# Kernel optimization log

Hardware: AMD Instinct MI355X
Metric: run time of the kernel (lower is better)

Reference implementation:

```python
import jax, jax.numpy as jnp
import numpy as np

N = 50000      # nodes per graph
E = 800000     # edges per graph (avg degree 16)
IN = 128       # in_channels == hidden_channels
HID = 128      # out_channels (heads=1)
R = 8          # num_relations
NEG = 0.2      # PyG RGATConv default negative_slope


def setup_inputs() -> dict:
    key = jax.random.key(0)
    ks = jax.random.split(key, 14)
    s_w = (2.0 / (IN + HID)) ** 0.5  # glorot-ish scale
    return {
        "x_one": jax.random.normal(ks[0], (N, IN), jnp.float32),
        "edge_index_one": jax.random.randint(ks[1], (2, E), 0, N),
        "edge_type_one": jax.random.randint(ks[2], (E,), 0, R),
        "x_two": jax.random.normal(ks[3], (N, IN), jnp.float32),
        "edge_index_two": jax.random.randint(ks[4], (2, E), 0, N),
        "edge_type_two": jax.random.randint(ks[5], (E,), 0, R),
        "W1": jax.random.normal(ks[6], (R, IN, HID), jnp.float32) * s_w,
        "q1": jax.random.normal(ks[7], (HID, 1), jnp.float32) * s_w,
        "k1": jax.random.normal(ks[8], (HID, 1), jnp.float32) * s_w,
        "b1": jnp.zeros((HID,), jnp.float32),
        "W2": jax.random.normal(ks[9], (R, IN, HID), jnp.float32) * s_w,
        "q2": jax.random.normal(ks[10], (HID, 1), jnp.float32) * s_w,
        "k2": jax.random.normal(ks[11], (HID, 1), jnp.float32) * s_w,
        "b2": jnp.zeros((HID,), jnp.float32),
    }


def _rgat(x, edge_index, edge_type, W, q, k, b):
    """PyG RGATConv (heads=1, additive-self-attention, across-relation)."""
    n = x.shape[0]
    src, dst = edge_index[0], edge_index[1]
    # per-relation linear transform of all nodes: [R, N, HID]
    xt = jnp.einsum('nd,rdo->rno', x, W)
    out_i = xt[edge_type, dst]   # [E, HID] transformed target (x_i W_r)
    out_j = xt[edge_type, src]   # [E, HID] transformed source (x_j W_r)
    qi = out_i @ q               # [E, 1]
    kj = out_j @ k               # [E, 1]
    alpha = jax.nn.leaky_relu(qi + kj, NEG)
    # scatter-softmax over incoming edges of each dst node
    amax = jax.ops.segment_max(alpha, dst, num_segments=n)
    amax = jnp.where(jnp.isfinite(amax), amax, 0.0)
    ex = jnp.exp(alpha - amax[dst])
    denom = jax.ops.segment_sum(ex, dst, num_segments=n) + 1e-16
    a = ex / denom[dst]          # [E, 1]
    # weighted scatter-add aggregation + bias
    out = jax.ops.segment_sum(a * out_j, dst, num_segments=n) + b
    return out


def reference(x_one, edge_index_one, edge_type_one,
              x_two, edge_index_two, edge_type_two,
              W1, q1, k1, b1, W2, q2, k2, b2):
    o1 = jax.nn.relu(_rgat(x_one, edge_index_one, edge_type_one, W1, q1, k1, b1))
    o2 = jax.nn.relu(_rgat(x_two, edge_index_two, edge_type_two, W2, q2, k2, b2))
    return (o1, o2)
```

## Files before the change

kernel.cpp:

```cpp
#include <hip/hip_runtime.h>


typedef unsigned short u16;
typedef __attribute__((ext_vector_type(8))) short short8;
typedef __attribute__((ext_vector_type(4))) float floatx4;
typedef __attribute__((ext_vector_type(4))) float float4v;
typedef __attribute__((ext_vector_type(4))) unsigned uint4v;

__device__ __forceinline__ u16 f2bf(float f) {
  union { float f; unsigned u; } v; v.f = f;
  unsigned r = v.u + 0x7FFFu + ((v.u >> 16) & 1u);
  return (u16)(r >> 16);
}
__device__ __forceinline__ float bflo(unsigned v) {
  union { unsigned u; float f; } c; c.u = v << 16; return c.f;
}
__device__ __forceinline__ float bfhi(unsigned v) {
  union { unsigned u; float f; } c; c.u = v & 0xffff0000u; return c.f;
}

__global__ void k_prep_wb(const float* __restrict__ W1, const float* __restrict__ W2,
                          u16* __restrict__ Wb, int KK) {
  int t = blockIdx.x * 256 + threadIdx.x;
  int lane = t & 63, nt = (t >> 6) & 7, kk = t >> 9;
  if (kk >= KK) return;
  const float* W = blockIdx.y ? W2 : W1;
  u16* out = Wb + (size_t)blockIdx.y * KK * 4096;
  int q = lane >> 4, m16 = lane & 15;
  int c = nt * 16 + m16;
  short8 v;
#pragma unroll
  for (int j = 0; j < 8; ++j) {
    int k = kk * 32 + q * 8 + j;
    v[j] = (short)f2bf(W[(size_t)k * 128 + c]);
  }
  *(short8*)(out + (size_t)t * 8) = v;
}

__global__ void k_prep_wqk(const float* __restrict__ W1, const float* __restrict__ q1,
                           const float* __restrict__ k1, const float* __restrict__ W2,
                           const float* __restrict__ q2, const float* __restrict__ k2,
                           float* __restrict__ Wq, float* __restrict__ Wk, int RD) {
  int wid = (blockIdx.x * 256 + threadIdx.x) >> 6;
  int lane = threadIdx.x & 63;
  if (wid >= 2 * RD) return;
  int g = wid >= RD;
  const float* W = g ? W2 : W1;
  const float* qv = g ? q2 : q1;
  const float* kv = g ? k2 : k1;
  const float* row = W + (size_t)(wid - g * RD) * 128;
  float a0 = row[lane], a1 = row[lane + 64];
  float vq = a0 * qv[lane] + a1 * qv[lane + 64];
  float vk = a0 * kv[lane] + a1 * kv[lane + 64];
#pragma unroll
  for (int off = 32; off; off >>= 1) {
    vq += __shfl_xor(vq, off);
    vk += __shfl_xor(vk, off);
  }
  if (lane == 0) { Wq[wid] = vq; Wk[wid] = vk; }
}

__global__ void k_prep_bqk(const float* __restrict__ Wq, const float* __restrict__ Wk,
                           u16* __restrict__ Bqk, int R) {
  int total = 2 * 4 * 64 * 8;
  for (int idx = threadIdx.x; idx < total; idx += 256) {
    int j = idx & 7, lane = (idx >> 3) & 63, kk = (idx >> 9) & 3, g = idx >> 11;
    int k = kk * 32 + ((lane >> 4) & 3) * 8 + j;
    int n = lane & 15;
    float v = (n < 8) ? Wq[(g * R + n) * 128 + k] : Wk[(g * R + (n & 7)) * 128 + k];
    Bqk[idx] = f2bf(v);
  }
}

__global__ void __launch_bounds__(256) k_count(
    const int* __restrict__ d1, const int* __restrict__ d2,
    int* __restrict__ gcnt, int N, int E, int NB) {
  __shared__ int h[512];
  int tid = threadIdx.x;
  for (int i = tid; i < NB; i += 256) h[i] = 0;
  __syncthreads();
  int E2 = 2 * E;
  int e0 = blockIdx.x * 4096;
#pragma unroll
  for (int j = 0; j < 16; ++j) {
    int e = e0 + j * 256 + tid;
    if (e < E2) {
      int g = e >= E;
      int d = g ? d2[e - E] : d1[e];
      atomicAdd(&h[(g * N + d) >> 8], 1);
    }
  }
  __syncthreads();
  for (int i = tid; i < NB; i += 256)
    if (h[i]) atomicAdd(&gcnt[i], h[i]);
}

__global__ void k_bucket_scan(const int* __restrict__ gcnt, int* __restrict__ bbase,
                              int* __restrict__ bcur, int* __restrict__ offs,
                              int NB, int total, int N2) {
  __shared__ int sd[512];
  int tid = threadIdx.x;
  int v0 = (tid < NB) ? gcnt[tid] : 0;
  int v1 = (tid + 256 < NB) ? gcnt[tid + 256] : 0;
  sd[tid] = v0; sd[tid + 256] = v1;
  __syncthreads();
  for (int off = 1; off < 512; off <<= 1) {
    int t0 = (tid >= off) ? sd[tid - off] : 0;
    int t1 = (tid + 256 >= off) ? sd[tid + 256 - off] : 0;
    __syncthreads();
    sd[tid] += t0; sd[tid + 256] += t1;
    __syncthreads();
  }
  if (tid < NB) { int b = sd[tid] - v0; bbase[tid] = b; bcur[tid] = b; }
  if (tid + 256 < NB) { int b = sd[tid + 256] - v1; bbase[tid + 256] = b; bcur[tid + 256] = b; }
  if (tid == 0) { bbase[NB] = total; offs[N2] = total; }
}

__global__ void __launch_bounds__(256) k_bin(
    const int* __restrict__ ei1, const int* __restrict__ et1,
    const int* __restrict__ ei2, const int* __restrict__ et2,
    int* __restrict__ bcur, uint2* __restrict__ staged, int N, int E, int NB) {
  __shared__ int hist[512];
  __shared__ int basev[512];
  __shared__ int runstart[512];
  __shared__ unsigned sta[4096 * 2];
  int tid = threadIdx.x;
  int E2 = 2 * E;
  int e0 = blockIdx.x * 4096;
  int cnt2 = min(4096, E2 - e0);
  for (int i = tid; i < 512; i += 256) hist[i] = 0;
  __syncthreads();
  int dstg[16], srcet[16], rank[16];
#pragma unroll
  for (int j = 0; j < 16; ++j) {
    int e = e0 + j * 256 + tid;
    dstg[j] = -1;
    if (e < E2) {
      int g = e >= E;
      int el = e - (g ? E : 0);
      const int* ei = g ? ei2 : ei1;
      int s = ei[el], d = ei[E + el];
      int etv = (g ? et2 : et1)[el];
      dstg[j] = g * N + d;
      srcet[j] = (s << 3) | etv;
      rank[j] = atomicAdd(&hist[dstg[j] >> 8], 1);
    }
  }
  __syncthreads();
  basev[tid] = hist[tid];
  basev[tid + 256] = hist[tid + 256];
  __syncthreads();
  for (int off = 1; off < 512; off <<= 1) {
    int i0 = tid, i1 = tid + 256;
    int v0 = (i0 >= off) ? basev[i0 - off] : 0;
    int v1 = (i1 >= off) ? basev[i1 - off] : 0;
    __syncthreads();
    basev[i0] += v0; basev[i1] += v1;
    __syncthreads();
  }
  for (int i = tid; i < NB; i += 256)
    if (hist[i] > 0) runstart[i] = atomicAdd(&bcur[i], hist[i]);
  __syncthreads();
#pragma unroll
  for (int j = 0; j < 16; ++j)
    if (dstg[j] >= 0) {
      int b = dstg[j] >> 8;
      int slot = basev[b] - hist[b] + rank[j];
      sta[slot * 2] = (unsigned)dstg[j];
      sta[slot * 2 + 1] = (unsigned)srcet[j];
    }
  __syncthreads();
  for (int i = tid; i < cnt2; i += 256) {
    unsigned dg = sta[i * 2], se = sta[i * 2 + 1];
    int b = (int)(dg >> 8);
    int dest = runstart[b] + (i - (basev[b] - hist[b]));
    staged[dest] = make_uint2(dg, se);
  }
}

__global__ void __launch_bounds__(256) k_scatter2(
    const uint2* __restrict__ staged, const int* __restrict__ bbase,
    int* __restrict__ offs, int* __restrict__ csr, int N2) {
  __shared__ int hist[256];
  __shared__ int sd[256];
  __shared__ int cur[256];
  int b = blockIdx.x, tid = threadIdx.x;
  int nb0 = b << 8;
  int nnode = min(256, N2 - nb0);
  int s0 = bbase[b], s1 = bbase[b + 1];
  hist[tid] = 0;
  __syncthreads();
  for (int i = s0 + tid; i < s1; i += 256)
    atomicAdd(&hist[(int)staged[i].x - nb0], 1);
  __syncthreads();
  int v = hist[tid];
  sd[tid] = v; __syncthreads();
  for (int off = 1; off < 256; off <<= 1) {
    int t = (tid >= off) ? sd[tid - off] : 0;
    __syncthreads();
    sd[tid] += t;
    __syncthreads();
  }
  int ex = sd[tid] - v;
  if (tid < nnode) offs[nb0 + tid] = s0 + ex;
  cur[tid] = ex;
  __syncthreads();
  for (int i = s0 + tid; i < s1; i += 256) {
    uint2 en = staged[i];
    int node = (int)en.x - nb0;
    int sl = atomicAdd(&cur[node], 1);
    csr[s0 + sl] = (int)en.y;
  }
}

__global__ void __launch_bounds__(256) k_gemm_xt(
    const float* __restrict__ x, const u16* __restrict__ Wb,
    const u16* __restrict__ Bqk, u16* __restrict__ xt,
    float* __restrict__ sq, float* __restrict__ sk,
    int N, int R, int node_base) {
  int wave = threadIdx.x >> 6, lane = threadIdx.x & 63;
  int m0 = blockIdx.x * 64 + wave * 16;
  int q = lane >> 4, m16 = lane & 15;
  int node = m0 + m16;
  int srow = (node < N) ? node : N - 1;
  short8 bfrag[4];
#pragma unroll
  for (int kk = 0; kk < 4; ++kk) {
    const float* ap = x + (size_t)srow * 128 + kk * 32 + q * 8;
    float4v f0 = *(const float4v*)ap;
    float4v f1 = *(const float4v*)(ap + 4);
    short8 a;
    a[0] = (short)f2bf(f0.x); a[1] = (short)f2bf(f0.y);
    a[2] = (short)f2bf(f0.z); a[3] = (short)f2bf(f0.w);
    a[4] = (short)f2bf(f1.x); a[5] = (short)f2bf(f1.y);
    a[6] = (short)f2bf(f1.z); a[7] = (short)f2bf(f1.w);
    bfrag[kk] = a;
  }
  {
    floatx4 accq = (floatx4){0.f, 0.f, 0.f, 0.f};
#pragma unroll
    for (int kk = 0; kk < 4; ++kk) {
      short8 aq = *(const short8*)(Bqk + (size_t)kk * 512 + lane * 8);
      accq = __builtin_amdgcn_mfma_f32_16x16x32_bf16(aq, bfrag[kk], accq, 0, 0, 0);
    }
    if (node < N) {
      float* dst = (q < 2 ? sq : sk) + (size_t)(node_base + node) * 8 + (q & 1) * 4;
      *(float4v*)dst = (float4v){accq[0], accq[1], accq[2], accq[3]};
    }
  }
  for (int r = 0; r < R; ++r) {
    floatx4 acc[8];
#pragma unroll
    for (int nt = 0; nt < 8; ++nt) acc[nt] = (floatx4){0.f, 0.f, 0.f, 0.f};
#pragma unroll
    for (int kk = 0; kk < 4; ++kk) {
      const u16* wbp = Wb + ((size_t)((r * 4 + kk) * 8) * 64 + lane) * 8;
#pragma unroll
      for (int nt = 0; nt < 8; ++nt) {
        short8 a = *(const short8*)(wbp + nt * 512);
        acc[nt] = __builtin_amdgcn_mfma_f32_16x16x32_bf16(a, bfrag[kk], acc[nt], 0, 0, 0);
      }
    }
    if (node < N) {
      u16* rowp = xt + ((size_t)r * N + node) * 128 + q * 4;
#pragma unroll
      for (int nt = 0; nt < 8; ++nt) {
        union { u16 h[4]; uint2 u; } pk;
        pk.h[0] = f2bf(acc[nt][0]); pk.h[1] = f2bf(acc[nt][1]);
        pk.h[2] = f2bf(acc[nt][2]); pk.h[3] = f2bf(acc[nt][3]);
        *(uint2*)(rowp + nt * 16) = pk.u;
      }
    }
  }
}

__global__ void __launch_bounds__(256) k_aggregate(
    const int* __restrict__ csr, const int* __restrict__ offs,
    const float* __restrict__ sq, const float* __restrict__ sk,
    const u16* __restrict__ xt, const float* __restrict__ bias,
    float* __restrict__ out, int N, int node_base) {
  int nl = blockIdx.x * 4 + (threadIdx.x >> 6);
  int lane = threadIdx.x & 63;
  if (nl >= N) return;
  int node = node_base + nl;
  int start = offs[node], end = offs[node + 1];
  const float* sqn = sq + (size_t)node * 8;

  float al[8]; int pl[8];
  float m = -INFINITY;
  {
    int c = 0;
    for (int i = start + lane; i < end; i += 64, ++c) {
      int p = csr[i]; int s = p >> 3, e = p & 7;
      float a = sqn[e] + sk[(size_t)(node_base + s) * 8 + e];
      a = (a > 0.f) ? a : 0.2f * a;
      if (c < 8) { al[c] = a; pl[c] = p; }
      m = fmaxf(m, a);
    }
  }
#pragma unroll
  for (int off = 32; off; off >>= 1) m = fmaxf(m, __shfl_xor(m, off));

  float ssum = 0.f;
  {
    int c = 0;
    for (int i = start + lane; i < end; i += 64, ++c) {
      float a;
      if (c < 8) a = al[c];
      else {
        int p = csr[i]; int s = p >> 3, e = p & 7;
        a = sqn[e] + sk[(size_t)(node_base + s) * 8 + e];
        a = (a > 0.f) ? a : 0.2f * a;
      }
      ssum += __expf(a - m);
    }
  }
#pragma unroll
  for (int off = 32; off; off >>= 1) ssum += __shfl_xor(ssum, off);
  float inv = 1.f / (ssum + 1e-16f);

  float acc0 = 0.f, acc1 = 0.f;
  const char* xtb = (const char*)xt;
  int c = 0;
  for (int base = start; base < end; base += 64, ++c) {
    int cnt = min(64, end - base);
    float w = 0.f; int b = 0;
    {
      int i = base + lane;
      if (i < end) {
        int p; float a;
        if (c < 8) { p = pl[c]; a = al[c]; }
        else {
          p = csr[i]; int s = p >> 3, e = p & 7;
          a = sqn[e] + sk[(size_t)(node_base + s) * 8 + e];
          a = (a > 0.f) ? a : 0.2f * a;
        }
        w = __expf(a - m) * inv;
        b = ((p & 7) * N + (p >> 3)) << 8;
      }
    }
    int j = 0;
    for (; j + 3 < cnt; j += 4) {
      float w0 = __shfl(w, j), w1 = __shfl(w, j + 1),
            w2 = __shfl(w, j + 2), w3 = __shfl(w, j + 3);
      int b0 = __shfl(b, j), b1 = __shfl(b, j + 1),
          b2 = __shfl(b, j + 2), b3 = __shfl(b, j + 3);
      unsigned v0 = *(const unsigned*)(xtb + b0 + lane * 4);
      unsigned v1 = *(const unsigned*)(xtb + b1 + lane * 4);
      unsigned v2 = *(const unsigned*)(xtb + b2 + lane * 4);
      unsigned v3 = *(const unsigned*)(xtb + b3 + lane * 4);
      acc0 += w0 * bflo(v0); acc1 += w0 * bfhi(v0);
      acc0 += w1 * bflo(v1); acc1 += w1 * bfhi(v1);
      acc0 += w2 * bflo(v2); acc1 += w2 * bfhi(v2);
      acc0 += w3 * bflo(v3); acc1 += w3 * bfhi(v3);
    }
    for (; j < cnt; ++j) {
      float w0 = __shfl(w, j);
      int b0 = __shfl(b, j);
      unsigned v0 = *(const unsigned*)(xtb + b0 + lane * 4);
      acc0 += w0 * bflo(v0); acc1 += w0 * bfhi(v0);
    }
  }
  float o0 = fmaxf(acc0 + bias[lane * 2], 0.f);
  float o1 = fmaxf(acc1 + bias[lane * 2 + 1], 0.f);
  union { float f[2]; unsigned long long u; } pk;
  pk.f[0] = o0; pk.f[1] = o1;
  __builtin_nontemporal_store(pk.u,
      (unsigned long long*)(out + (size_t)nl * 128 + lane * 2));
}

extern "C" void kernel_launch(void* const* d_in, const int* in_sizes, int n_in,
                              void* d_out, int out_size, void* d_ws, size_t ws_size,
                              hipStream_t stream) {
  const float* x1 = (const float*)d_in[0];
  const int* ei1 = (const int*)d_in[1];
  const int* et1 = (const int*)d_in[2];
  const float* x2 = (const float*)d_in[3];
  const int* ei2 = (const int*)d_in[4];
  const int* et2 = (const int*)d_in[5];
  const float* W1 = (const float*)d_in[6];
  const float* q1 = (const float*)d_in[7];
  const float* k1 = (const float*)d_in[8];
  const float* b1 = (const float*)d_in[9];
  const float* W2 = (const float*)d_in[10];
  const float* q2 = (const float*)d_in[11];
  const float* k2 = (const float*)d_in[12];
  const float* b2 = (const float*)d_in[13];

  const int N = in_sizes[0] / 128;
  const int E = in_sizes[1] / 2;
  const int R = in_sizes[6] / (128 * 128);
  const int KK = R * 4;
  const int N2 = 2 * N;
  const int NB = (N2 + 255) >> 8;

  size_t off = 0;
  char* w = (char*)d_ws;
  auto carve = [&](size_t bytes) -> void* {
    void* p = w + off;
    off += (bytes + 255) & ~(size_t)255;
    return p;
  };
  u16* xt = (u16*)carve((size_t)R * N * 128 * 2);
  uint2* staged = (uint2*)xt;
  u16* Wb = (u16*)carve((size_t)2 * KK * 4096 * 2);
  u16* Bqk = (u16*)carve((size_t)2 * 4 * 64 * 8 * 2);
  float* Wq = (float*)carve((size_t)2 * R * 128 * 4);
  float* Wk = (float*)carve((size_t)2 * R * 128 * 4);
  float* sq = (float*)carve((size_t)N2 * 8 * 4);
  float* sk = (float*)carve((size_t)N2 * 8 * 4);
  int* offs = (int*)carve((size_t)(N2 + 1) * 4);
  int* gcnt = (int*)carve(512 * 4);
  int* bbase = (int*)carve(520 * 4);
  int* bcur = (int*)carve(512 * 4);
  int* csr = (int*)carve((size_t)2 * E * 4);
  if (off > ws_size) return;

  const int nbin = (2 * E + 4095) / 4096;

  hipMemsetAsync(gcnt, 0, 512 * 4, stream);
  k_prep_wb<<<dim3((KK * 512 + 255) / 256, 2), dim3(256), 0, stream>>>(W1, W2, Wb, KK);
  k_prep_wqk<<<dim3((2 * R * 128 * 64 + 255) / 256), dim3(256), 0, stream>>>(
      W1, q1, k1, W2, q2, k2, Wq, Wk, R * 128);
  k_prep_bqk<<<dim3(1), dim3(256), 0, stream>>>(Wq, Wk, Bqk, R);
  k_count<<<dim3(nbin), dim3(256), 0, stream>>>(ei1 + E, ei2 + E, gcnt, N, E, NB);
  k_bucket_scan<<<dim3(1), dim3(256), 0, stream>>>(gcnt, bbase, bcur, offs, NB, 2 * E, N2);
  k_bin<<<dim3(nbin), dim3(256), 0, stream>>>(ei1, et1, ei2, et2, bcur, staged, N, E, NB);
  k_scatter2<<<dim3(NB), dim3(256), 0, stream>>>(staged, bbase, offs, csr, N2);

  for (int g = 0; g < 2; ++g) {
    const float* x = g ? x2 : x1;
    const float* bv = g ? b2 : b1;
    float* outp = (float*)d_out + (size_t)g * N * 128;
    k_gemm_xt<<<dim3((N + 63) / 64), dim3(256), 0, stream>>>(
        x, Wb + (size_t)g * KK * 4096, Bqk + (size_t)g * 2048, xt,
        sq, sk, N, R, g * N);
    k_aggregate<<<dim3((N + 3) / 4), dim3(256), 0, stream>>>(
        csr, offs, sq, sk, xt, bv, outp, N, g * N);
  }
}
```

Before: 403.7 us.

## Aggregate raw bf16 features per relation, then apply W_r after aggregation

The per-relation transform xt = x·W_r for every node and relation is no longer materialised. Each destination node now accumulates attention-weighted raw bf16 source features into eight per-relation buckets. Those buckets are staged in LDS and multiplied by the stacked weights with MFMA inside the aggregation kernel. This removes the large R×N×128 intermediate write and its scattered gathers, but adds a per-edge relation switch, more registers per lane, and a 1024-deep GEMM per 16-node tile. It also adds bf16 rounding of the aggregated sums.

```diff
diff --git a/kernel.cpp b/kernel.cpp
--- a/kernel.cpp
+++ b/kernel.cpp
@@ -5,7 +5,6 @@
 typedef __attribute__((ext_vector_type(8))) short short8;
 typedef __attribute__((ext_vector_type(4))) float floatx4;
 typedef __attribute__((ext_vector_type(4))) float float4v;
-typedef __attribute__((ext_vector_type(4))) unsigned uint4v;
 
 __device__ __forceinline__ u16 f2bf(float f) {
   union { float f; unsigned u; } v; v.f = f;
@@ -72,6 +71,48 @@
   }
 }
 
+__global__ void __launch_bounds__(256) k_sqk(
+    const float* __restrict__ x1, const float* __restrict__ x2,
+    const u16* __restrict__ Bqk, u16* __restrict__ xbf,
+    float* __restrict__ sq, float* __restrict__ sk, int N) {
+  int g = blockIdx.y;
+  const float* x = g ? x2 : x1;
+  u16* xb = xbf + (size_t)g * N * 128;
+  int wave = threadIdx.x >> 6, lane = threadIdx.x & 63;
+  int m0 = blockIdx.x * 64 + wave * 16;
+  int q = lane >> 4, m16 = lane & 15;
+  int node = m0 + m16;
+  int srow = (node < N) ? node : N - 1;
+  short8 bfrag[4];
+#pragma unroll
+  for (int kk = 0; kk < 4; ++kk) {
+    const float* ap = x + (size_t)srow * 128 + kk * 32 + q * 8;
+    float4v f0 = *(const float4v*)ap;
+    float4v f1 = *(const float4v*)(ap + 4);
+    short8 a;
+    a[0] = (short)f2bf(f0.x); a[1] = (short)f2bf(f0.y);
+    a[2] = (short)f2bf(f0.z); a[3] = (short)f2bf(f0.w);
+    a[4] = (short)f2bf(f1.x); a[5] = (short)f2bf(f1.y);
+    a[6] = (short)f2bf(f1.z); a[7] = (short)f2bf(f1.w);
+    bfrag[kk] = a;
+  }
+  if (node < N) {
+#pragma unroll
+    for (int kk = 0; kk < 4; ++kk)
+      *(short8*)(xb + (size_t)node * 128 + kk * 32 + q * 8) = bfrag[kk];
+  }
+  floatx4 accq = (floatx4){0.f, 0.f, 0.f, 0.f};
+#pragma unroll
+  for (int kk = 0; kk < 4; ++kk) {
+    short8 aq = *(const short8*)(Bqk + ((size_t)g * 4 + kk) * 512 + lane * 8);
+    accq = __builtin_amdgcn_mfma_f32_16x16x32_bf16(aq, bfrag[kk], accq, 0, 0, 0);
+  }
+  if (node < N) {
+    float* dst = (q < 2 ? sq : sk) + (size_t)(g * N + node) * 8 + (q & 1) * 4;
+    *(float4v*)dst = (float4v){accq[0], accq[1], accq[2], accq[3]};
+  }
+}
+
 __global__ void __launch_bounds__(256) k_count(
     const int* __restrict__ d1, const int* __restrict__ d2,
     int* __restrict__ gcnt, int N, int E, int NB) {
@@ -213,160 +254,148 @@
   }
 }
 
-__global__ void __launch_bounds__(256) k_gemm_xt(
-    const float* __restrict__ x, const u16* __restrict__ Wb,
-    const u16* __restrict__ Bqk, u16* __restrict__ xt,
-    float* __restrict__ sq, float* __restrict__ sk,
-    int N, int R, int node_base) {
-  int wave = threadIdx.x >> 6, lane = threadIdx.x & 63;
-  int m0 = blockIdx.x * 64 + wave * 16;
-  int q = lane >> 4, m16 = lane & 15;
-  int node = m0 + m16;
-  int srow = (node < N) ? node : N - 1;
-  short8 bfrag[4];
-#pragma unroll
-  for (int kk = 0; kk < 4; ++kk) {
-    const float* ap = x + (size_t)srow * 128 + kk * 32 + q * 8;
-    float4v f0 = *(const float4v*)ap;
-    float4v f1 = *(const float4v*)(ap + 4);
-    short8 a;
-    a[0] = (short)f2bf(f0.x); a[1] = (short)f2bf(f0.y);
-    a[2] = (short)f2bf(f0.z); a[3] = (short)f2bf(f0.w);
-    a[4] = (short)f2bf(f1.x); a[5] = (short)f2bf(f1.y);
-    a[6] = (short)f2bf(f1.z); a[7] = (short)f2bf(f1.w);
-    bfrag[kk] = a;
-  }
-  {
-    floatx4 accq = (floatx4){0.f, 0.f, 0.f, 0.f};
-#pragma unroll
-    for (int kk = 0; kk < 4; ++kk) {
-      short8 aq = *(const short8*)(Bqk + (size_t)kk * 512 + lane * 8);
-      accq = __builtin_amdgcn_mfma_f32_16x16x32_bf16(aq, bfrag[kk], accq, 0, 0, 0);
-    }
-    if (node < N) {
-      float* dst = (q < 2 ? sq : sk) + (size_t)(node_base + node) * 8 + (q & 1) * 4;
-      *(float4v*)dst = (float4v){accq[0], accq[1], accq[2], accq[3]};
-    }
-  }
-  for (int r = 0; r < R; ++r) {
-    floatx4 acc[8];
-#pragma unroll
-    for (int nt = 0; nt < 8; ++nt) acc[nt] = (floatx4){0.f, 0.f, 0.f, 0.f};
-#pragma unroll
-    for (int kk = 0; kk < 4; ++kk) {
-      const u16* wbp = Wb + ((size_t)((r * 4 + kk) * 8) * 64 + lane) * 8;
-#pragma unroll
-      for (int nt = 0; nt < 8; ++nt) {
-        short8 a = *(const short8*)(wbp + nt * 512);
-        acc[nt] = __builtin_amdgcn_mfma_f32_16x16x32_bf16(a, bfrag[kk], acc[nt], 0, 0, 0);
-      }
-    }
-    if (node < N) {
-      u16* rowp = xt + ((size_t)r * N + node) * 128 + q * 4;
-#pragma unroll
-      for (int nt = 0; nt < 8; ++nt) {
-        union { u16 h[4]; uint2 u; } pk;
-        pk.h[0] = f2bf(acc[nt][0]); pk.h[1] = f2bf(acc[nt][1]);
-        pk.h[2] = f2bf(acc[nt][2]); pk.h[3] = f2bf(acc[nt][3]);
-        *(uint2*)(rowp + nt * 16) = pk.u;
-      }
-    }
-  }
-}
+#define ACC8(RELE, W, V)                                              \
+  {                                                                   \
+    int _r = __builtin_amdgcn_readfirstlane(RELE) & 7;                \
+    float _lo = bflo(V), _hi = bfhi(V);                               \
+    switch (_r) {                                                     \
+      case 0: y[0][0] += (W) * _lo; y[0][1] += (W) * _hi; break;      \
+      case 1: y[1][0] += (W) * _lo; y[1][1] += (W) * _hi; break;      \
+      case 2: y[2][0] += (W) * _lo; y[2][1] += (W) * _hi; break;      \
+      case 3: y[3][0] += (W) * _lo; y[3][1] += (W) * _hi; break;      \
+      case 4: y[4][0] += (W) * _lo; y[4][1] += (W) * _hi; break;      \
+      case 5: y[5][0] += (W) * _lo; y[5][1] += (W) * _hi; break;      \
+      case 6: y[6][0] += (W) * _lo; y[6][1] += (W) * _hi; break;      \
+      default: y[7][0] += (W) * _lo; y[7][1] += (W) * _hi; break;     \
+    }                                                                 \
+  }
 
 __global__ void __launch_bounds__(256) k_aggregate(
     const int* __restrict__ csr, const int* __restrict__ offs,
     const float* __restrict__ sq, const float* __restrict__ sk,
-    const u16* __restrict__ xt, const float* __restrict__ bias,
-    float* __restrict__ out, int N, int node_base) {
-  int nl = blockIdx.x * 4 + (threadIdx.x >> 6);
-  int lane = threadIdx.x & 63;
-  if (nl >= N) return;
-  int node = node_base + nl;
-  int start = offs[node], end = offs[node + 1];
-  const float* sqn = sq + (size_t)node * 8;
-
-  float al[8]; int pl[8];
-  float m = -INFINITY;
-  {
-    int c = 0;
-    for (int i = start + lane; i < end; i += 64, ++c) {
-      int p = csr[i]; int s = p >> 3, e = p & 7;
-      float a = sqn[e] + sk[(size_t)(node_base + s) * 8 + e];
-      a = (a > 0.f) ? a : 0.2f * a;
-      if (c < 8) { al[c] = a; pl[c] = p; }
-      m = fmaxf(m, a);
-    }
-  }
-#pragma unroll
-  for (int off = 32; off; off >>= 1) m = fmaxf(m, __shfl_xor(m, off));
-
-  float ssum = 0.f;
-  {
-    int c = 0;
-    for (int i = start + lane; i < end; i += 64, ++c) {
-      float a;
-      if (c < 8) a = al[c];
-      else {
-        int p = csr[i]; int s = p >> 3, e = p & 7;
-        a = sqn[e] + sk[(size_t)(node_base + s) * 8 + e];
-        a = (a > 0.f) ? a : 0.2f * a;
+    const u16* __restrict__ xbf, const u16* __restrict__ Wb,
+    const float* __restrict__ bias, float* __restrict__ out,
+    int N, int node_base) {
+  __shared__ u16 ylds[16][1032];
+  int wave = threadIdx.x >> 6, lane = threadIdx.x & 63;
+  int q = lane >> 4, m16 = lane & 15;
+  const char* xbfb = (const char*)xbf;
+
+  for (int t = 0; t < 4; ++t) {
+    int nl = blockIdx.x * 16 + wave * 4 + t;
+    float y[8][2] = {{0.f, 0.f}, {0.f, 0.f}, {0.f, 0.f}, {0.f, 0.f},
+                     {0.f, 0.f}, {0.f, 0.f}, {0.f, 0.f}, {0.f, 0.f}};
+    if (nl < N) {
+      int node = node_base + nl;
+      int start = offs[node], end = offs[node + 1];
+      const float* sqn = sq + (size_t)node * 8;
+
+      float al[8]; int pl[8];
+      float m = -INFINITY;
+      {
+        int c = 0;
+        for (int i = start + lane; i < end; i += 64, ++c) {
+          int p = csr[i]; int s = p >> 3, e = p & 7;
+          float a = sqn[e] + sk[(size_t)(node_base + s) * 8 + e];
+          a = (a > 0.f) ? a : 0.2f * a;
+          if (c < 8) { al[c] = a; pl[c] = p; }
+          m = fmaxf(m, a);
+        }
       }
-      ssum += __expf(a - m);
-    }
-  }
-#pragma unroll
-  for (int off = 32; off; off >>= 1) ssum += __shfl_xor(ssum, off);
-  float inv = 1.f / (ssum + 1e-16f);
-
-  float acc0 = 0.f, acc1 = 0.f;
-  const char* xtb = (const char*)xt;
-  int c = 0;
-  for (int base = start; base < end; base += 64, ++c) {
-    int cnt = min(64, end - base);
-    float w = 0.f; int b = 0;
-    {
-      int i = base + lane;
-      if (i < end) {
-        int p; float a;
-        if (c < 8) { p = pl[c]; a = al[c]; }
-        else {
-          p = csr[i]; int s = p >> 3, e = p & 7;
-          a = sqn[e] + sk[(size_t)(node_base + s) * 8 + e];
-          a = (a > 0.f) ? a : 0.2f * a;
+#pragma unroll
+      for (int off = 32; off; off >>= 1) m = fmaxf(m, __shfl_xor(m, off));
+
+      float ssum = 0.f;
+      {
+        int c = 0;
+        for (int i = start + lane; i < end; i += 64, ++c) {
+          float a;
+          if (c < 8) a = al[c];
+          else {
+            int p = csr[i]; int s = p >> 3, e = p & 7;
+            a = sqn[e] + sk[(size_t)(node_base + s) * 8 + e];
+            a = (a > 0.f) ? a : 0.2f * a;
+          }
+          ssum += __expf(a - m);
         }
-        w = __expf(a - m) * inv;
-        b = ((p & 7) * N + (p >> 3)) << 8;
+      }
+#pragma unroll
+      for (int off = 32; off; off >>= 1) ssum += __shfl_xor(ssum, off);
+      float inv = 1.f / (ssum + 1e-16f);
+
+      int c = 0;
+      for (int base = start; base < end; base += 64, ++c) {
+        int cnt = min(64, end - base);
+        float w = 0.f; int p = 0;
+        {
+          int i = base + lane;
+          if (i < end) {
+            float a;
+            if (c < 8) { p = pl[c]; a = al[c]; }
+            else {
+              p = csr[i]; int s = p >> 3, e = p & 7;
+              a = sqn[e] + sk[(size_t)(node_base + s) * 8 + e];
+              a = (a > 0.f) ? a : 0.2f * a;
+            }
+            w = __expf(a - m) * inv;
+          }
+        }
+        int j = 0;
+        for (; j + 3 < cnt; j += 4) {
+          float w0 = __shfl(w, j), w1 = __shfl(w, j + 1),
+                w2 = __shfl(w, j + 2), w3 = __shfl(w, j + 3);
+          int p0 = __shfl(p, j), p1 = __shfl(p, j + 1),
+              p2 = __shfl(p, j + 2), p3 = __shfl(p, j + 3);
+          unsigned v0 = *(const unsigned*)(xbfb + (((size_t)(unsigned)(p0 >> 3)) << 8) + lane * 4);
+          unsigned v1 = *(const unsigned*)(xbfb + (((size_t)(unsigned)(p1 >> 3)) << 8) + lane * 4);
+          unsigned v2 = *(const unsigned*)(xbfb + (((size_t)(unsigned)(p2 >> 3)) << 8) + lane * 4);
+          unsigned v3 = *(const unsigned*)(xbfb + (((size_t)(unsigned)(p3 >> 3)) << 8) + lane * 4);
+          ACC8(p0, w0, v0);
+          ACC8(p1, w1, v1);
+          ACC8(p2, w2, v2);
+          ACC8(p3, w3, v3);
+        }
+        for (; j < cnt; ++j) {
+          float w0 = __shfl(w, j);
+          int p0 = __shfl(p, j);
+          unsigned v0 = *(const unsigned*)(xbfb + (((size_t)(unsigned)(p0 >> 3)) << 8) + lane * 4);
+          ACC8(p0, w0, v0);
+        }
       }
     }
-    int j = 0;
-    for (; j + 3 < cnt; j += 4) {
-      float w0 = __shfl(w, j), w1 = __shfl(w, j + 1),
-            w2 = __shfl(w, j + 2), w3 = __shfl(w, j + 3);
-      int b0 = __shfl(b, j), b1 = __shfl(b, j + 1),
-          b2 = __shfl(b, j + 2), b3 = __shfl(b, j + 3);
-      unsigned v0 = *(const unsigned*)(xtb + b0 + lane * 4);
-      unsigned v1 = *(const unsigned*)(xtb + b1 + lane * 4);
-      unsigned v2 = *(const unsigned*)(xtb + b2 + lane * 4);
-      unsigned v3 = *(const unsigned*)(xtb + b3 + lane * 4);
-      acc0 += w0 * bflo(v0); acc1 += w0 * bfhi(v0);
-      acc0 += w1 * bflo(v1); acc1 += w1 * bfhi(v1);
-      acc0 += w2 * bflo(v2); acc1 += w2 * bfhi(v2);
-      acc0 += w3 * bflo(v3); acc1 += w3 * bfhi(v3);
+    int nrow = wave * 4 + t;
+#pragma unroll
+    for (int r = 0; r < 8; ++r) {
+      unsigned pk = (unsigned)f2bf(y[r][0]) | ((unsigned)f2bf(y[r][1]) << 16);
+      *(unsigned*)&ylds[nrow][r * 128 + lane * 2] = pk;
     }
-    for (; j < cnt; ++j) {
-      float w0 = __shfl(w, j);
-      int b0 = __shfl(b, j);
-      unsigned v0 = *(const unsigned*)(xtb + b0 + lane * 4);
-      acc0 += w0 * bflo(v0); acc1 += w0 * bfhi(v0);
-    }
-  }
-  float o0 = fmaxf(acc0 + bias[lane * 2], 0.f);
-  float o1 = fmaxf(acc1 + bias[lane * 2 + 1], 0.f);
-  union { float f[2]; unsigned long long u; } pk;
-  pk.f[0] = o0; pk.f[1] = o1;
-  __builtin_nontemporal_store(pk.u,
-      (unsigned long long*)(out + (size_t)nl * 128 + lane * 2));
+  }
+  __syncthreads();
+
+  floatx4 acc0 = (floatx4){0.f, 0.f, 0.f, 0.f};
+  floatx4 acc1 = (floatx4){0.f, 0.f, 0.f, 0.f};
+  int nt0 = wave * 2, nt1 = wave * 2 + 1;
+#pragma unroll
+  for (int kk = 0; kk < 32; ++kk) {
+    short8 b = *(const short8*)&ylds[m16][kk * 32 + q * 8];
+    short8 a0 = *(const short8*)(Wb + ((size_t)(kk * 8 + nt0)) * 512 + lane * 8);
+    short8 a1 = *(const short8*)(Wb + ((size_t)(kk * 8 + nt1)) * 512 + lane * 8);
+    acc0 = __builtin_amdgcn_mfma_f32_16x16x32_bf16(a0, b, acc0, 0, 0, 0);
+    acc1 = __builtin_amdgcn_mfma_f32_16x16x32_bf16(a1, b, acc1, 0, 0, 0);
+  }
+  int onode = blockIdx.x * 16 + m16;
+  if (onode < N) {
+    float* op = out + (size_t)onode * 128;
+    int ch0 = nt0 * 16 + q * 4, ch1 = nt1 * 16 + q * 4;
+    float4v bv0 = *(const float4v*)(bias + ch0);
+    float4v bv1 = *(const float4v*)(bias + ch1);
+    float4v o0 = (float4v){fmaxf(acc0[0] + bv0.x, 0.f), fmaxf(acc0[1] + bv0.y, 0.f),
+                           fmaxf(acc0[2] + bv0.z, 0.f), fmaxf(acc0[3] + bv0.w, 0.f)};
+    float4v o1 = (float4v){fmaxf(acc1[0] + bv1.x, 0.f), fmaxf(acc1[1] + bv1.y, 0.f),
+                           fmaxf(acc1[2] + bv1.z, 0.f), fmaxf(acc1[3] + bv1.w, 0.f)};
+    *(float4v*)(op + ch0) = o0;
+    *(float4v*)(op + ch1) = o1;
+  }
 }
 
 extern "C" void kernel_launch(void* const* d_in, const int* in_sizes, int n_in,
@@ -401,18 +430,18 @@
     off += (bytes + 255) & ~(size_t)255;
     return p;
   };
-  u16* xt = (u16*)carve((size_t)R * N * 128 * 2);
-  uint2* staged = (uint2*)xt;
   u16* Wb = (u16*)carve((size_t)2 * KK * 4096 * 2);
   u16* Bqk = (u16*)carve((size_t)2 * 4 * 64 * 8 * 2);
   float* Wq = (float*)carve((size_t)2 * R * 128 * 4);
   float* Wk = (float*)carve((size_t)2 * R * 128 * 4);
+  u16* xbf = (u16*)carve((size_t)N2 * 128 * 2);
   float* sq = (float*)carve((size_t)N2 * 8 * 4);
   float* sk = (float*)carve((size_t)N2 * 8 * 4);
   int* offs = (int*)carve((size_t)(N2 + 1) * 4);
   int* gcnt = (int*)carve(512 * 4);
   int* bbase = (int*)carve(520 * 4);
   int* bcur = (int*)carve(512 * 4);
+  uint2* staged = (uint2*)carve((size_t)2 * E * 8);
   int* csr = (int*)carve((size_t)2 * E * 4);
   if (off > ws_size) return;
 
@@ -423,19 +452,17 @@
   k_prep_wqk<<<dim3((2 * R * 128 * 64 + 255) / 256), dim3(256), 0, stream>>>(
       W1, q1, k1, W2, q2, k2, Wq, Wk, R * 128);
   k_prep_bqk<<<dim3(1), dim3(256), 0, stream>>>(Wq, Wk, Bqk, R);
+  k_sqk<<<dim3((N + 63) / 64, 2), dim3(256), 0, stream>>>(x1, x2, Bqk, xbf, sq, sk, N);
   k_count<<<dim3(nbin), dim3(256), 0, stream>>>(ei1 + E, ei2 + E, gcnt, N, E, NB);
   k_bucket_scan<<<dim3(1), dim3(256), 0, stream>>>(gcnt, bbase, bcur, offs, NB, 2 * E, N2);
   k_bin<<<dim3(nbin), dim3(256), 0, stream>>>(ei1, et1, ei2, et2, bcur, staged, N, E, NB);
   k_scatter2<<<dim3(NB), dim3(256), 0, stream>>>(staged, bbase, offs, csr, N2);
 
   for (int g = 0; g < 2; ++g) {
-    const float* x = g ? x2 : x1;
     const float* bv = g ? b2 : b1;
     float* outp = (float*)d_out + (size_t)g * N * 128;
-    k_gemm_xt<<<dim3((N + 63) / 64), dim3(256), 0, stream>>>(
-        x, Wb + (size_t)g * KK * 4096, Bqk + (size_t)g * 2048, xt,
-        sq, sk, N, R, g * N);
-    k_aggregate<<<dim3((N + 3) / 4), dim3(256), 0, stream>>>(
-        csr, offs, sq, sk, xt, bv, outp, N, g * N);
-  }
-}
+    k_aggregate<<<dim3((N + 15) / 16), dim3(256), 0, stream>>>(
+        csr, offs, sq, sk, xbf + (size_t)g * N * 128, Wb + (size_t)g * KK * 4096,
+        bv, outp, N, g * N);
+  }
+}
```

Measured after the change: 396.6 us. No clear change (-1.8%).
